# Performance work log

Measured on AMD Instinct MI355X. Metric: run time of the kernel, lower is better.

The kernel has to match this reference:

```python
import jax, jax.numpy as jnp
import numpy as np

# Fixed LeNet C3 connection table: input channel i feeds these 10 output channels.
CONN = [[0, 4, 5, 6, 9, 10, 11, 12, 14, 15],
        [0, 1, 5, 6, 7, 10, 11, 12, 13, 15],
        [0, 1, 2, 6, 7, 8, 11, 13, 14, 15],
        [1, 2, 3, 6, 7, 8, 9, 12, 14, 15],
        [2, 3, 4, 7, 8, 9, 10, 12, 13, 15],
        [3, 4, 5, 8, 9, 10, 11, 13, 14, 15]]
# Static scatter indices: (out_channel, in_channel) pairs, 60 total.
_ROWS = np.concatenate([np.asarray(l, np.int32) for l in CONN])  # out-channel ids
_COLS = np.repeat(np.arange(6, dtype=np.int32), 10)              # in-channel ids


def setup_inputs() -> dict:
    key = jax.random.key(0)
    k1, k2 = jax.random.split(key)
    x = jax.random.normal(k1, (64, 6, 256, 256), jnp.float32)
    # kaiming-uniform-ish scale for 6*5*5 fan-in
    weight = jax.random.normal(k2, (10, 6, 5, 5), jnp.float32) * 0.1
    bias = jnp.full((1, 16, 1, 1), 0.01, jnp.float32)
    return {"x": x, "weight": weight, "bias": bias}


def reference(x, weight, bias):
    # Fold the per-input-channel loop + scatter-add into one dense [16,6,5,5]
    # kernel with zeros where the connection table is absent. Each iteration i
    # of the original adds conv(x[:,i], weight[j,i]) to out channel CONN[i][j].
    w_flat = weight.transpose(1, 0, 2, 3).reshape(60, 5, 5)  # ordered (i, j)
    w_full = jnp.zeros((16, 6, 5, 5), weight.dtype).at[_ROWS, _COLS].set(w_flat)
    # Bias for channel c is added once per list containing c -> multiply by count.
    counts = jnp.zeros((16,), weight.dtype).at[_ROWS].add(1.0)
    out = jax.lax.conv_general_dilated(
        x, w_full, window_strides=(1, 1), padding='VALID',
        dimension_numbers=('NCHW', 'OIHW', 'NCHW'))
    return out + bias * counts.reshape(1, 16, 1, 1)
```

## Files before the change

### kernel.cpp

```cpp
#include <hip/hip_runtime.h>
#include <hip/hip_fp16.h>

typedef _Float16 f16x8 __attribute__((ext_vector_type(8)));
typedef float f32x16 __attribute__((ext_vector_type(16)));

__device__ constexpr int CONN[6][10] = {
    {0, 4, 5, 6, 9, 10, 11, 12, 14, 15},
    {0, 1, 5, 6, 7, 10, 11, 12, 13, 15},
    {0, 1, 2, 6, 7, 8, 11, 13, 14, 15},
    {1, 2, 3, 6, 7, 8, 9, 12, 14, 15},
    {2, 3, 4, 7, 8, 9, 10, 12, 13, 15},
    {3, 4, 5, 8, 9, 10, 11, 13, 14, 15}};

__device__ constexpr int CNT[16] = {3,3,3,3,3,3,4,4,4,4,4,4,4,4,4,6};

__device__ __forceinline__ f16x8 u4_to_h8(uint4 u) { f16x8 r; __builtin_memcpy(&r, &u, 16); return r; }

#define PITCH_DW 132
#define PLANE_DW 2128
#define LDS_DW   (6 * 2128 + 140)

__global__ void prep_A(const float* __restrict__ w, unsigned short* __restrict__ Wp) {
    int t = blockIdx.x * 256 + threadIdx.x;
    if (t >= 7680) return;
    int j = t & 7, lane = (t >> 3) & 63, ms = t >> 9;
    int ch = lane & 31, kb = lane >> 5;
    int slice = ms + 15 * kb;
    int ii = slice / 5, r = slice % 5;
    float val = 0.f;
    if (ch < 16 && j < 5)
        for (int jj = 0; jj < 10; ++jj)
            if (CONN[ii][jj] == ch) val = w[jj * 150 + ii * 25 + r * 5 + j];
    __half h = __float2half(val);
    unsigned short u; __builtin_memcpy(&u, &h, 2);
    Wp[t] = u;
}

__global__ __launch_bounds__(256, 2) void c3_mfma(
    const float* __restrict__ x, const unsigned short* __restrict__ Wp,
    const float* __restrict__ bias, float* __restrict__ out)
{
    __shared__ unsigned s_lds[LDS_DW];

    const int tid = threadIdx.x;
    const int id = (blockIdx.x & 7) * 168 + (blockIdx.x >> 3);
    const int by = id % 21;
    const int n  = id / 21;
    const int Y0 = by * 12;
    const float* xin = x + (size_t)n * 6 * 65536;

    #pragma unroll 4
    for (int it = 0; it < 24; ++it) {
        int i   = tid + it * 256;
        int c4  = i & 63;
        int row = (i >> 6) & 15;
        int ch  = i >> 10;
        float4 v = *reinterpret_cast<const float4*>(
            xin + (size_t)ch * 65536 + (size_t)(Y0 + row) * 256 + c4 * 4);
        __half2 lo = __floats2half2_rn(v.x, v.y);
        __half2 hi = __floats2half2_rn(v.z, v.w);
        uint2 u; __builtin_memcpy(&u.x, &lo, 4); __builtin_memcpy(&u.y, &hi, 4);
        *reinterpret_cast<uint2*>(&s_lds[ch * PLANE_DW + row * PITCH_DW + c4 * 2]) = u;
    }
    if (tid < 96) {
        int ch = tid >> 4, row = tid & 15;
        *reinterpret_cast<uint4*>(&s_lds[ch * PLANE_DW + row * PITCH_DW + 128]) =
            make_uint4(0u, 0u, 0u, 0u);
    }
    __syncthreads();

    const int lane = tid & 63;
    const int wv   = tid >> 6;
    const int nn   = lane & 31;
    const int kb   = lane >> 5;

    f16x8 W[15];
    const uint4* wp4 = reinterpret_cast<const uint4*>(Wp);
    #pragma unroll
    for (int ms = 0; ms < 15; ++ms) W[ms] = u4_to_h8(wp4[ms * 64 + lane]);

    f32x16 cinit;
    #pragma unroll
    for (int reg = 0; reg < 8; ++reg) {
        int ch = (reg & 3) + 8 * (reg >> 2) + 4 * kb;
        cinit[reg] = bias[ch] * (float)CNT[ch];
    }
    #pragma unroll
    for (int reg = 8; reg < 16; ++reg) cinit[reg] = 0.f;

    const int gxL = 32 * wv + nn;
    const int gxH = 128 + 32 * wv + nn;
    const bool okH = gxH < 252;
    const int pbL = 3 * kb * PLANE_DW + (gxL >> 1);
    const int pbH = 3 * kb * PLANE_DW + (gxH >> 1);
    const bool oddL = (gxL >> 1) & 1;
    const bool oddH = (gxH >> 1) & 1;
    const unsigned shb = (unsigned)((nn & 1) * 16);

    auto loadf = [&](int dw, bool odd) -> f16x8 {
        int d0 = dw & ~1;
        uint2 r0 = *reinterpret_cast<const uint2*>(&s_lds[d0]);
        uint2 r1 = *reinterpret_cast<const uint2*>(&s_lds[d0 + 2]);
        uint2 r2 = *reinterpret_cast<const uint2*>(&s_lds[d0 + 4]);
        unsigned e0 = odd ? r0.y : r0.x;
        unsigned e1 = odd ? r1.x : r0.y;
        unsigned e2 = odd ? r1.y : r1.x;
        unsigned e3 = odd ? r2.x : r1.y;
        unsigned e4 = odd ? r2.y : r2.x;
        unsigned o0 = (unsigned)((((unsigned long long)e1 << 32) | e0) >> shb);
        unsigned o1 = (unsigned)((((unsigned long long)e2 << 32) | e1) >> shb);
        unsigned o2 = (unsigned)((((unsigned long long)e3 << 32) | e2) >> shb);
        unsigned o3 = (unsigned)((((unsigned long long)e4 << 32) | e3) >> shb);
        return u4_to_h8(make_uint4(o0, o1, o2, o3));
    };

    f16x8 L00 = loadf(pbL + 0*PITCH_DW, oddL), L01 = loadf(pbL + 1*PITCH_DW, oddL),
          L02 = loadf(pbL + 2*PITCH_DW, oddL), L03 = loadf(pbL + 3*PITCH_DW, oddL),
          L04 = loadf(pbL + 4*PITCH_DW, oddL);
    f16x8 L10 = loadf(pbL + PLANE_DW + 0*PITCH_DW, oddL), L11 = loadf(pbL + PLANE_DW + 1*PITCH_DW, oddL),
          L12 = loadf(pbL + PLANE_DW + 2*PITCH_DW, oddL), L13 = loadf(pbL + PLANE_DW + 3*PITCH_DW, oddL),
          L14 = loadf(pbL + PLANE_DW + 4*PITCH_DW, oddL);
    f16x8 L20 = loadf(pbL + 2*PLANE_DW + 0*PITCH_DW, oddL), L21 = loadf(pbL + 2*PLANE_DW + 1*PITCH_DW, oddL),
          L22 = loadf(pbL + 2*PLANE_DW + 2*PITCH_DW, oddL), L23 = loadf(pbL + 2*PLANE_DW + 3*PITCH_DW, oddL),
          L24 = loadf(pbL + 2*PLANE_DW + 4*PITCH_DW, oddL);
    f16x8 H00 = loadf(pbH + 0*PITCH_DW, oddH), H01 = loadf(pbH + 1*PITCH_DW, oddH),
          H02 = loadf(pbH + 2*PITCH_DW, oddH), H03 = loadf(pbH + 3*PITCH_DW, oddH),
          H04 = loadf(pbH + 4*PITCH_DW, oddH);
    f16x8 H10 = loadf(pbH + PLANE_DW + 0*PITCH_DW, oddH), H11 = loadf(pbH + PLANE_DW + 1*PITCH_DW, oddH),
          H12 = loadf(pbH + PLANE_DW + 2*PITCH_DW, oddH), H13 = loadf(pbH + PLANE_DW + 3*PITCH_DW, oddH),
          H14 = loadf(pbH + PLANE_DW + 4*PITCH_DW, oddH);
    f16x8 H20 = loadf(pbH + 2*PLANE_DW + 0*PITCH_DW, oddH), H21 = loadf(pbH + 2*PLANE_DW + 1*PITCH_DW, oddH),
          H22 = loadf(pbH + 2*PLANE_DW + 2*PITCH_DW, oddH), H23 = loadf(pbH + 2*PLANE_DW + 3*PITCH_DW, oddH),
          H24 = loadf(pbH + 2*PLANE_DW + 4*PITCH_DW, oddH);
    int rowOff = 5 * PITCH_DW;

    float* const opL = out + (size_t)n * 16 * 63504 + (size_t)(4 * kb) * 63504 + gxL;
    float* const opH = out + (size_t)n * 16 * 63504 + (size_t)(4 * kb) * 63504 + gxH;
    int yoff = Y0 * 252;

#define MFMA32(a, b, c) __builtin_amdgcn_mfma_f32_32x32x16_f16(a, b, c, 0, 0, 0)

#define STRIP(f00,f01,f02,f03,f04, f10,f11,f12,f13,f14, f20,f21,f22,f23,f24, pb, od, opg, ok) \
    {                                                                          \
        f32x16 acc = cinit;                                                    \
        acc = MFMA32(W[0],  f00, acc);  acc = MFMA32(W[1],  f01, acc);         \
        acc = MFMA32(W[2],  f02, acc);  acc = MFMA32(W[3],  f03, acc);         \
        acc = MFMA32(W[4],  f04, acc);                                         \
        acc = MFMA32(W[5],  f10, acc);  acc = MFMA32(W[6],  f11, acc);         \
        acc = MFMA32(W[7],  f12, acc);  acc = MFMA32(W[8],  f13, acc);         \
        acc = MFMA32(W[9],  f14, acc);                                         \
        acc = MFMA32(W[10], f20, acc);  acc = MFMA32(W[11], f21, acc);         \
        acc = MFMA32(W[12], f22, acc);  acc = MFMA32(W[13], f23, acc);         \
        acc = MFMA32(W[14], f24, acc);                                         \
        if (ok) {                                                              \
            opg[yoff +  0 * 63504] = acc[0];                                   \
            opg[yoff +  1 * 63504] = acc[1];                                   \
            opg[yoff +  2 * 63504] = acc[2];                                   \
            opg[yoff +  3 * 63504] = acc[3];                                   \
            opg[yoff +  8 * 63504] = acc[4];                                   \
            opg[yoff +  9 * 63504] = acc[5];                                   \
            opg[yoff + 10 * 63504] = acc[6];                                   \
            opg[yoff + 11 * 63504] = acc[7];                                   \
        }                                                                      \
        f00 = loadf(pb + rowOff, od);                                          \
        f10 = loadf(pb + PLANE_DW + rowOff, od);                               \
        f20 = loadf(pb + 2 * PLANE_DW + rowOff, od);                           \
    }

#define PHASE(r0,r1,r2,r3,r4)                                                          \
    STRIP(L0##r0,L0##r1,L0##r2,L0##r3,L0##r4, L1##r0,L1##r1,L1##r2,L1##r3,L1##r4,      \
          L2##r0,L2##r1,L2##r2,L2##r3,L2##r4, pbL, oddL, opL, true)                    \
    STRIP(H0##r0,H0##r1,H0##r2,H0##r3,H0##r4, H1##r0,H1##r1,H1##r2,H1##r3,H1##r4,      \
          H2##r0,H2##r1,H2##r2,H2##r3,H2##r4, pbH, oddH, opH, okH)                     \
    rowOff += PITCH_DW; yoff += 252;

    PHASE(0,1,2,3,4)
    PHASE(1,2,3,4,0)
    PHASE(2,3,4,0,1)
    PHASE(3,4,0,1,2)
    PHASE(4,0,1,2,3)
    PHASE(0,1,2,3,4)
    PHASE(1,2,3,4,0)
    PHASE(2,3,4,0,1)
    PHASE(3,4,0,1,2)
    PHASE(4,0,1,2,3)
    PHASE(0,1,2,3,4)
    PHASE(1,2,3,4,0)
#undef PHASE
#undef STRIP
#undef MFMA32
}

extern "C" void kernel_launch(void* const* d_in, const int* in_sizes, int n_in,
                              void* d_out, int out_size, void* d_ws, size_t ws_size,
                              hipStream_t stream) {
    const float* x    = (const float*)d_in[0];
    const float* w    = (const float*)d_in[1];
    const float* bias = (const float*)d_in[2];
    float* out = (float*)d_out;
    unsigned short* Wp = (unsigned short*)d_ws;

    hipLaunchKernelGGL(prep_A, dim3(30), dim3(256), 0, stream, w, Wp);
    hipLaunchKernelGGL(c3_mfma, dim3(1344), dim3(256), 0, stream, x, Wp, bias, out);
}
```

Measured before the change: 105.0 us.

## Fuse weight packing into conv kernel, interleave MFMA chains, drop LDS padding

Removes the separate prep_A launch: each block now builds the packed fp16 weight panel in shared memory itself, then loads its weight registers from LDS instead of a global workspace. The low and high column strips now run as two interleaved accumulator chains, so independent MFMAs can hide each other's latency. The LDS row pitch drops from 132 to 128 dwords and the zero-pad column is gone, so edge loads read into the next row. Those reads only feed outputs already masked by okH. The trade-off is redundant weight-packing work and extra global weight reads in every one of the 1344 blocks, plus possible LDS bank conflicts from the power-of-two pitch.

```diff
diff --git a/kernel.cpp b/kernel.cpp
--- a/kernel.cpp
+++ b/kernel.cpp
@@ -16,31 +16,17 @@
 
 __device__ __forceinline__ f16x8 u4_to_h8(uint4 u) { f16x8 r; __builtin_memcpy(&r, &u, 16); return r; }
 
-#define PITCH_DW 132
-#define PLANE_DW 2128
-#define LDS_DW   (6 * 2128 + 140)
-
-__global__ void prep_A(const float* __restrict__ w, unsigned short* __restrict__ Wp) {
-    int t = blockIdx.x * 256 + threadIdx.x;
-    if (t >= 7680) return;
-    int j = t & 7, lane = (t >> 3) & 63, ms = t >> 9;
-    int ch = lane & 31, kb = lane >> 5;
-    int slice = ms + 15 * kb;
-    int ii = slice / 5, r = slice % 5;
-    float val = 0.f;
-    if (ch < 16 && j < 5)
-        for (int jj = 0; jj < 10; ++jj)
-            if (CONN[ii][jj] == ch) val = w[jj * 150 + ii * 25 + r * 5 + j];
-    __half h = __float2half(val);
-    unsigned short u; __builtin_memcpy(&u, &h, 2);
-    Wp[t] = u;
-}
+#define PITCH_DW 128
+#define PLANE_DW 2048
+#define PANEL_DW 12288
+#define LDS_DW   16128
 
 __global__ __launch_bounds__(256, 2) void c3_mfma(
-    const float* __restrict__ x, const unsigned short* __restrict__ Wp,
+    const float* __restrict__ x, const float* __restrict__ w,
     const float* __restrict__ bias, float* __restrict__ out)
 {
     __shared__ unsigned s_lds[LDS_DW];
+    unsigned short* s_panel = reinterpret_cast<unsigned short*>(s_lds + PANEL_DW);
 
     const int tid = threadIdx.x;
     const int id = (blockIdx.x & 7) * 168 + (blockIdx.x >> 3);
@@ -48,6 +34,20 @@
     const int n  = id / 21;
     const int Y0 = by * 12;
     const float* xin = x + (size_t)n * 6 * 65536;
+
+    for (int t = tid; t < 7680; t += 256) {
+        int j = t & 7, lane = (t >> 3) & 63, ms = t >> 9;
+        int ch = lane & 31, kb = lane >> 5;
+        int slice = ms + 15 * kb;
+        int ii = slice / 5, r = slice % 5;
+        float val = 0.f;
+        if (ch < 16 && j < 5)
+            for (int jj = 0; jj < 10; ++jj)
+                if (CONN[ii][jj] == ch) val = w[jj * 150 + ii * 25 + r * 5 + j];
+        __half h = __float2half(val);
+        unsigned short u; __builtin_memcpy(&u, &h, 2);
+        s_panel[t] = u;
+    }
 
     #pragma unroll 4
     for (int it = 0; it < 24; ++it) {
@@ -62,11 +62,6 @@
         uint2 u; __builtin_memcpy(&u.x, &lo, 4); __builtin_memcpy(&u.y, &hi, 4);
         *reinterpret_cast<uint2*>(&s_lds[ch * PLANE_DW + row * PITCH_DW + c4 * 2]) = u;
     }
-    if (tid < 96) {
-        int ch = tid >> 4, row = tid & 15;
-        *reinterpret_cast<uint4*>(&s_lds[ch * PLANE_DW + row * PITCH_DW + 128]) =
-            make_uint4(0u, 0u, 0u, 0u);
-    }
     __syncthreads();
 
     const int lane = tid & 63;
@@ -75,9 +70,11 @@
     const int kb   = lane >> 5;
 
     f16x8 W[15];
-    const uint4* wp4 = reinterpret_cast<const uint4*>(Wp);
-    #pragma unroll
-    for (int ms = 0; ms < 15; ++ms) W[ms] = u4_to_h8(wp4[ms * 64 + lane]);
+    {
+        const uint4* p4 = reinterpret_cast<const uint4*>(s_panel);
+        #pragma unroll
+        for (int ms = 0; ms < 15; ++ms) W[ms] = u4_to_h8(p4[ms * 64 + lane]);
+    }
 
     f32x16 cinit;
     #pragma unroll
@@ -89,7 +86,7 @@
     for (int reg = 8; reg < 16; ++reg) cinit[reg] = 0.f;
 
     const int gxL = 32 * wv + nn;
-    const int gxH = 128 + 32 * wv + nn;
+    const int gxH = 128 + gxL;
     const bool okH = gxH < 252;
     const int pbL = 3 * kb * PLANE_DW + (gxL >> 1);
     const int pbH = 3 * kb * PLANE_DW + (gxH >> 1);
@@ -135,59 +132,77 @@
     int rowOff = 5 * PITCH_DW;
 
     float* const opL = out + (size_t)n * 16 * 63504 + (size_t)(4 * kb) * 63504 + gxL;
-    float* const opH = out + (size_t)n * 16 * 63504 + (size_t)(4 * kb) * 63504 + gxH;
+    float* const opH = opL + 128;
     int yoff = Y0 * 252;
 
 #define MFMA32(a, b, c) __builtin_amdgcn_mfma_f32_32x32x16_f16(a, b, c, 0, 0, 0)
 
-#define STRIP(f00,f01,f02,f03,f04, f10,f11,f12,f13,f14, f20,f21,f22,f23,f24, pb, od, opg, ok) \
+#define PHASE(l00,l01,l02,l03,l04, l10,l11,l12,l13,l14, l20,l21,l22,l23,l24,   \
+              h00,h01,h02,h03,h04, h10,h11,h12,h13,h14, h20,h21,h22,h23,h24)   \
     {                                                                          \
-        f32x16 acc = cinit;                                                    \
-        acc = MFMA32(W[0],  f00, acc);  acc = MFMA32(W[1],  f01, acc);         \
-        acc = MFMA32(W[2],  f02, acc);  acc = MFMA32(W[3],  f03, acc);         \
-        acc = MFMA32(W[4],  f04, acc);                                         \
-        acc = MFMA32(W[5],  f10, acc);  acc = MFMA32(W[6],  f11, acc);         \
-        acc = MFMA32(W[7],  f12, acc);  acc = MFMA32(W[8],  f13, acc);         \
-        acc = MFMA32(W[9],  f14, acc);                                         \
-        acc = MFMA32(W[10], f20, acc);  acc = MFMA32(W[11], f21, acc);         \
-        acc = MFMA32(W[12], f22, acc);  acc = MFMA32(W[13], f23, acc);         \
-        acc = MFMA32(W[14], f24, acc);                                         \
-        if (ok) {                                                              \
-            opg[yoff +  0 * 63504] = acc[0];                                   \
-            opg[yoff +  1 * 63504] = acc[1];                                   \
-            opg[yoff +  2 * 63504] = acc[2];                                   \
-            opg[yoff +  3 * 63504] = acc[3];                                   \
-            opg[yoff +  8 * 63504] = acc[4];                                   \
-            opg[yoff +  9 * 63504] = acc[5];                                   \
-            opg[yoff + 10 * 63504] = acc[6];                                   \
-            opg[yoff + 11 * 63504] = acc[7];                                   \
+        f32x16 accL = cinit, accH = cinit;                                     \
+        accL = MFMA32(W[0],  l00, accL);  accH = MFMA32(W[0],  h00, accH);     \
+        accL = MFMA32(W[1],  l01, accL);  accH = MFMA32(W[1],  h01, accH);     \
+        accL = MFMA32(W[2],  l02, accL);  accH = MFMA32(W[2],  h02, accH);     \
+        accL = MFMA32(W[3],  l03, accL);  accH = MFMA32(W[3],  h03, accH);     \
+        accL = MFMA32(W[4],  l04, accL);  accH = MFMA32(W[4],  h04, accH);     \
+        accL = MFMA32(W[5],  l10, accL);  accH = MFMA32(W[5],  h10, accH);     \
+        accL = MFMA32(W[6],  l11, accL);  accH = MFMA32(W[6],  h11, accH);     \
+        accL = MFMA32(W[7],  l12, accL);  accH = MFMA32(W[7],  h12, accH);     \
+        accL = MFMA32(W[8],  l13, accL);  accH = MFMA32(W[8],  h13, accH);     \
+        accL = MFMA32(W[9],  l14, accL);  accH = MFMA32(W[9],  h14, accH);     \
+        accL = MFMA32(W[10], l20, accL);  accH = MFMA32(W[10], h20, accH);     \
+        accL = MFMA32(W[11], l21, accL);  accH = MFMA32(W[11], h21, accH);     \
+        accL = MFMA32(W[12], l22, accL);  accH = MFMA32(W[12], h22, accH);     \
+        accL = MFMA32(W[13], l23, accL);  accH = MFMA32(W[13], h23, accH);     \
+        accL = MFMA32(W[14], l24, accL);  accH = MFMA32(W[14], h24, accH);     \
+        opL[yoff +  0 * 63504] = accL[0];                                      \
+        opL[yoff +  1 * 63504] = accL[1];                                      \
+        opL[yoff +  2 * 63504] = accL[2];                                      \
+        opL[yoff +  3 * 63504] = accL[3];                                      \
+        opL[yoff +  8 * 63504] = accL[4];                                      \
+        opL[yoff +  9 * 63504] = accL[5];                                      \
+        opL[yoff + 10 * 63504] = accL[6];                                      \
+        opL[yoff + 11 * 63504] = accL[7];                                      \
+        if (okH) {                                                             \
+            opH[yoff +  0 * 63504] = accH[0];                                  \
+            opH[yoff +  1 * 63504] = accH[1];                                  \
+            opH[yoff +  2 * 63504] = accH[2];                                  \
+            opH[yoff +  3 * 63504] = accH[3];                                  \
+            opH[yoff +  8 * 63504] = accH[4];                                  \
+            opH[yoff +  9 * 63504] = accH[5];                                  \
+            opH[yoff + 10 * 63504] = accH[6];                                  \
+            opH[yoff + 11 * 63504] = accH[7];                                  \
         }                                                                      \
-        f00 = loadf(pb + rowOff, od);                                          \
-        f10 = loadf(pb + PLANE_DW + rowOff, od);                               \
-        f20 = loadf(pb + 2 * PLANE_DW + rowOff, od);                           \
-    }
-
-#define PHASE(r0,r1,r2,r3,r4)                                                          \
-    STRIP(L0##r0,L0##r1,L0##r2,L0##r3,L0##r4, L1##r0,L1##r1,L1##r2,L1##r3,L1##r4,      \
-          L2##r0,L2##r1,L2##r2,L2##r3,L2##r4, pbL, oddL, opL, true)                    \
-    STRIP(H0##r0,H0##r1,H0##r2,H0##r3,H0##r4, H1##r0,H1##r1,H1##r2,H1##r3,H1##r4,      \
-          H2##r0,H2##r1,H2##r2,H2##r3,H2##r4, pbH, oddH, opH, okH)                     \
-    rowOff += PITCH_DW; yoff += 252;
-
-    PHASE(0,1,2,3,4)
-    PHASE(1,2,3,4,0)
-    PHASE(2,3,4,0,1)
-    PHASE(3,4,0,1,2)
-    PHASE(4,0,1,2,3)
-    PHASE(0,1,2,3,4)
-    PHASE(1,2,3,4,0)
-    PHASE(2,3,4,0,1)
-    PHASE(3,4,0,1,2)
-    PHASE(4,0,1,2,3)
-    PHASE(0,1,2,3,4)
-    PHASE(1,2,3,4,0)
+        l00 = loadf(pbL + rowOff, oddL);                                       \
+        l10 = loadf(pbL + PLANE_DW + rowOff, oddL);                            \
+        l20 = loadf(pbL + 2 * PLANE_DW + rowOff, oddL);                        \
+        h00 = loadf(pbH + rowOff, oddH);                                       \
+        h10 = loadf(pbH + PLANE_DW + rowOff, oddH);                            \
+        h20 = loadf(pbH + 2 * PLANE_DW + rowOff, oddH);                        \
+        rowOff += PITCH_DW; yoff += 252;                                       \
+    }
+
+#define P(r0,r1,r2,r3,r4)                                                              \
+    PHASE(L0##r0,L0##r1,L0##r2,L0##r3,L0##r4, L1##r0,L1##r1,L1##r2,L1##r3,L1##r4,      \
+          L2##r0,L2##r1,L2##r2,L2##r3,L2##r4,                                          \
+          H0##r0,H0##r1,H0##r2,H0##r3,H0##r4, H1##r0,H1##r1,H1##r2,H1##r3,H1##r4,      \
+          H2##r0,H2##r1,H2##r2,H2##r3,H2##r4)
+
+    P(0,1,2,3,4)
+    P(1,2,3,4,0)
+    P(2,3,4,0,1)
+    P(3,4,0,1,2)
+    P(4,0,1,2,3)
+    P(0,1,2,3,4)
+    P(1,2,3,4,0)
+    P(2,3,4,0,1)
+    P(3,4,0,1,2)
+    P(4,0,1,2,3)
+    P(0,1,2,3,4)
+    P(1,2,3,4,0)
+#undef P
 #undef PHASE
-#undef STRIP
 #undef MFMA32
 }
 
@@ -198,8 +213,6 @@
     const float* w    = (const float*)d_in[1];
     const float* bias = (const float*)d_in[2];
     float* out = (float*)d_out;
-    unsigned short* Wp = (unsigned short*)d_ws;
-
-    hipLaunchKernelGGL(prep_A, dim3(30), dim3(256), 0, stream, w, Wp);
-    hipLaunchKernelGGL(c3_mfma, dim3(1344), dim3(256), 0, stream, x, Wp, bias, out);
+
+    hipLaunchKernelGGL(c3_mfma, dim3(1344), dim3(256), 0, stream, x, w, bias, out);
 }
```

After: 196.0 us. 1.87x slower.
